# Kernel optimization log

Measured on AMD Instinct MI355X. Metric: run time of the kernel, lower is better.

The kernel has to match this reference:

```python
import jax, jax.numpy as jnp
import numpy as np

B, T, D, H = 32, 1024, 256, 256


def setup_inputs() -> dict:
    key = jax.random.key(0)
    ks = jax.random.split(key, 11)
    x = jax.random.normal(ks[0], (B, T, D), dtype=jnp.float32)
    len_x = jax.random.randint(ks[1], (B,), 1, T + 1).astype(jnp.int32)

    def xavier(k, fan_in, fan_out):
        return (jax.random.normal(k, (fan_out, fan_in)) * np.sqrt(2.0 / (fan_in + fan_out))).astype(jnp.float32)

    def unif(k, fan_in, shape):
        bound = 1.0 / np.sqrt(fan_in)
        return jax.random.uniform(k, shape, minval=-bound, maxval=bound).astype(jnp.float32)

    return {
        "x": x, "len_x": len_x,
        "Ww1_w": xavier(ks[2], D, H), "Ww1_b": unif(ks[3], D, (H,)),
        "Ww2_w": unif(ks[4], H, (D, H)), "Ww2_b": unif(ks[5], H, (D,)),
        "Wb1_w": xavier(ks[6], D, H), "Wb1_b": unif(ks[7], D, (H,)),
        "Wb2_w": unif(ks[8], H, (D, H)), "Wb2_b": unif(ks[9], H, (D,)),
    }


def _mlp(c, w1, b1, w2, b2):
    h = jax.nn.gelu(c @ w1.T + b1, approximate=False)
    return h @ w2.T + b2


def _ragged_dft(z, lengths, inverse):
    # z: [B, T, D] complex64; per-sample DFT over the first lengths[i] steps.
    t = z.shape[1]
    n = jnp.arange(t)
    kn = (n[:, None] * n[None, :]).astype(jnp.float32)          # [T, T]
    l = lengths.astype(jnp.float32)[:, None, None]               # [B, 1, 1]
    sign = 1.0 if inverse else -1.0
    ang = sign * 2.0 * jnp.pi * kn[None, :, :] / l               # [B, T, T]
    valid = n[None, :] < lengths[:, None]                        # [B, T]
    mask = (valid[:, :, None] & valid[:, None, :]).astype(jnp.float32)
    Wm = jnp.exp(1j * ang).astype(jnp.complex64) * mask
    if inverse:
        Wm = Wm / l.astype(jnp.complex64)
    return jnp.einsum("bkn,bnd->bkd", Wm, z)


def _crelu(z):
    mag = jnp.abs(z)
    phase = jnp.angle(z)
    recomposed = (mag * jnp.exp(1j * phase)).astype(jnp.complex64)
    return jnp.where(mag > 0, recomposed, jnp.zeros((), jnp.complex64))


def reference(x, len_x, Ww1_w, Ww1_b, Ww2_w, Ww2_b, Wb1_w, Wb1_b, Wb2_w, Wb2_b):
    # mean over valid length (torch sums over full T; padding assumed zero-filled contributes)
    c = jnp.sum(x, axis=1) / len_x.astype(x.dtype)[:, None]      # [B, D]
    x_freq = _ragged_dft(x.astype(jnp.complex64), len_x, inverse=False)
    W = _mlp(c, Ww1_w, Ww1_b, Ww2_w, Ww2_b).astype(jnp.complex64)  # [B, D]
    b = _mlp(c, Wb1_w, Wb1_b, Wb2_w, Wb2_b).astype(jnp.complex64)  # [B, D]
    filtered = x_freq * (1.0 + W[:, None, :]) + b[:, None, :]
    activated = _crelu(filtered)
    x_recon = _ragged_dft(activated, len_x, inverse=True)
    return x_recon.real.astype(x.dtype)
```

## Files before the change

### kernel.cpp

```cpp
#include <hip/hip_runtime.h>
#include <math.h>

#define BB 32
#define TT 1024
#define DD 256
#define NBLK1 1024
#define CHUNKS_PER_B 32


__global__ __launch_bounds__(256)
void k_partial(const float* __restrict__ x, float* __restrict__ partial) {
    __shared__ float4 red[4][64];
    const int g    = blockIdx.x;
    const int tid  = threadIdx.x;
    const int wave = tid >> 6;
    const int lane = tid & 63;
    const int row0 = g * 32;

    const float4* xr = (const float4*)(x + (size_t)(row0 + wave * 8) * DD);
    float4 s; s.x = 0.f; s.y = 0.f; s.z = 0.f; s.w = 0.f;
#pragma unroll
    for (int r = 0; r < 8; ++r) {
        float4 v = xr[(size_t)r * 64 + lane];
        s.x += v.x; s.y += v.y; s.z += v.z; s.w += v.w;
    }
    red[wave][lane] = s;
    __syncthreads();
    if (tid < 64) {
        float4 a = red[0][tid], b = red[1][tid], c = red[2][tid], d = red[3][tid];
        float4 o;
        o.x = (a.x + b.x) + (c.x + d.x);
        o.y = (a.y + b.y) + (c.y + d.y);
        o.z = (a.z + b.z) + (c.z + d.z);
        o.w = (a.w + b.w) + (c.w + d.w);
        ((float4*)(partial + (size_t)g * DD))[tid] = o;
    }
}

__global__ __launch_bounds__(256)
void k_mlp(const float* __restrict__ partial, const int* __restrict__ len,
           const float* __restrict__ Ww1_w, const float* __restrict__ Ww1_b,
           const float* __restrict__ Ww2_w, const float* __restrict__ Ww2_b,
           const float* __restrict__ Wb1_w, const float* __restrict__ Wb1_b,
           const float* __restrict__ Wb2_w, const float* __restrict__ Wb2_b,
           float* __restrict__ Wout, float* __restrict__ Bout) {
    __shared__ float csh[DD];
    __shared__ float hsh[DD];
    const int tid = threadIdx.x;
    const int b   = blockIdx.x >> 1;
    const int mlp = blockIdx.x & 1;

    {
        float s = 0.f;
        const float* pp = partial + (size_t)(b * CHUNKS_PER_B) * DD + tid;
#pragma unroll
        for (int ch = 0; ch < CHUNKS_PER_B; ++ch) s += pp[(size_t)ch * DD];
        csh[tid] = s / (float)len[b];
    }
    __syncthreads();
    const float* w1 = mlp ? Wb1_w : Ww1_w;
    const float* b1 = mlp ? Wb1_b : Ww1_b;
    const float* w2 = mlp ? Wb2_w : Ww2_w;
    const float* b2 = mlp ? Wb2_b : Ww2_b;
    float* op       = mlp ? Bout  : Wout;
    {
        const float4* wr = (const float4*)(w1 + (size_t)tid * DD);
        const float4* cc = (const float4*)csh;
        float s = 0.f;
#pragma unroll 8
        for (int k = 0; k < 64; ++k) {
            float4 w = wr[k];
            float4 c4 = cc[k];
            s += w.x * c4.x + w.y * c4.y + w.z * c4.z + w.w * c4.w;
        }
        float v = s + b1[tid];
        hsh[tid] = 0.5f * v * (1.0f + erff(v * 0.70710678118654752440f));
    }
    __syncthreads();
    {
        const float4* wr = (const float4*)(w2 + (size_t)tid * DD);
        const float4* hh = (const float4*)hsh;
        float s = 0.f;
#pragma unroll 8
        for (int k = 0; k < 64; ++k) {
            float4 w = wr[k];
            float4 h4 = hh[k];
            s += w.x * h4.x + w.y * h4.y + w.z * h4.z + w.w * h4.w;
        }
        op[b * DD + tid] = s + b2[tid];
    }
}

__global__ __launch_bounds__(256)
void k_apply(const float* __restrict__ x, const int* __restrict__ len,
             const float* __restrict__ Wf, const float* __restrict__ Bf,
             float* __restrict__ out) {
    const int row  = blockIdx.x * 4 + (threadIdx.x >> 6);
    const int lane = threadIdx.x & 63;
    const int b = row >> 10;
    const int t = row & (TT - 1);
    const int L = len[b];
    const size_t base = (size_t)row * DD;
    float4* o4 = (float4*)(out + base);
    if (t >= L) {
        float4 z; z.x = 0.f; z.y = 0.f; z.z = 0.f; z.w = 0.f;
        o4[lane] = z;
        return;
    }
    float4 x4 = ((const float4*)(x + base))[lane];
    float4 w4 = ((const float4*)(Wf + b * DD))[lane];
    float4 r;
    r.x = x4.x + w4.x * x4.x;
    r.y = x4.y + w4.y * x4.y;
    r.z = x4.z + w4.z * x4.z;
    r.w = x4.w + w4.w * x4.w;
    if (t == 0) {
        float4 b4 = ((const float4*)(Bf + b * DD))[lane];
        r.x += b4.x; r.y += b4.y; r.z += b4.z; r.w += b4.w;
    }
    o4[lane] = r;
}

extern "C" void kernel_launch(void* const* d_in, const int* in_sizes, int n_in,
                              void* d_out, int out_size, void* d_ws, size_t ws_size,
                              hipStream_t stream) {
    const float* x     = (const float*)d_in[0];
    const int*   len   = (const int*)d_in[1];
    const float* Ww1_w = (const float*)d_in[2];
    const float* Ww1_b = (const float*)d_in[3];
    const float* Ww2_w = (const float*)d_in[4];
    const float* Ww2_b = (const float*)d_in[5];
    const float* Wb1_w = (const float*)d_in[6];
    const float* Wb1_b = (const float*)d_in[7];
    const float* Wb2_w = (const float*)d_in[8];
    const float* Wb2_b = (const float*)d_in[9];
    float* out = (float*)d_out;

    float* ws      = (float*)d_ws;
    float* partial = ws;
    float* Wout    = ws + 262144;
    float* Bout    = ws + 270336;

    k_partial<<<NBLK1, 256, 0, stream>>>(x, partial);
    k_mlp<<<2 * BB, 256, 0, stream>>>(partial, len,
                                      Ww1_w, Ww1_b, Ww2_w, Ww2_b,
                                      Wb1_w, Wb1_b, Wb2_w, Wb2_b,
                                      Wout, Bout);
    k_apply<<<BB * TT / 4, 256, 0, stream>>>(x, len, Wout, Bout, out);
}
```

Baseline: 119.7 us.

## Fuse partial column sums and MLP into one kernel via flag-based inter-block sync

Merges the per-chunk reduction kernel and the MLP kernel into a single launch. Every block writes its partial sum and publishes a tagged release flag. Selected blocks (two per batch) then spin on the flags of their 32 source chunks, acquire, and run the MLP. This removes one kernel launch and its gap. In exchange it relies on all waited-on blocks being co-resident or scheduled in order, and the flags are never reset, so later calls can see stale flags from a previous run.

```diff
diff --git a/kernel.cpp b/kernel.cpp
--- a/kernel.cpp
+++ b/kernel.cpp
@@ -5,57 +5,76 @@
 #define TT 1024
 #define DD 256
 #define NBLK1 1024
-#define CHUNKS_PER_B 32
+#define CHB 32
+
+#define TAGP 0x13570000u
 
 
-__global__ __launch_bounds__(256)
-void k_partial(const float* __restrict__ x, float* __restrict__ partial) {
+__global__ __launch_bounds__(256, 4)
+void k_partial_mlp(const float* __restrict__ x, const int* __restrict__ len,
+                   const float* __restrict__ Ww1_w, const float* __restrict__ Ww1_b,
+                   const float* __restrict__ Ww2_w, const float* __restrict__ Ww2_b,
+                   const float* __restrict__ Wb1_w, const float* __restrict__ Wb1_b,
+                   const float* __restrict__ Wb2_w, const float* __restrict__ Wb2_b,
+                   float* __restrict__ partial,
+                   unsigned* __restrict__ pflag,
+                   float* __restrict__ Wout,
+                   float* __restrict__ Bout)
+{
     __shared__ float4 red[4][64];
+    __shared__ float  csh[DD];
+    __shared__ float  hsh[DD];
+
     const int g    = blockIdx.x;
     const int tid  = threadIdx.x;
     const int wave = tid >> 6;
     const int lane = tid & 63;
     const int row0 = g * 32;
 
-    const float4* xr = (const float4*)(x + (size_t)(row0 + wave * 8) * DD);
-    float4 s; s.x = 0.f; s.y = 0.f; s.z = 0.f; s.w = 0.f;
+    {
+        const float4* xr = (const float4*)(x + (size_t)(row0 + wave * 8) * DD);
+        float4 s; s.x = 0.f; s.y = 0.f; s.z = 0.f; s.w = 0.f;
 #pragma unroll
-    for (int r = 0; r < 8; ++r) {
-        float4 v = xr[(size_t)r * 64 + lane];
-        s.x += v.x; s.y += v.y; s.z += v.z; s.w += v.w;
+        for (int r = 0; r < 8; ++r) {
+            float4 v = xr[(size_t)r * 64 + lane];
+            s.x += v.x; s.y += v.y; s.z += v.z; s.w += v.w;
+        }
+        red[wave][lane] = s;
     }
-    red[wave][lane] = s;
     __syncthreads();
     if (tid < 64) {
-        float4 a = red[0][tid], b = red[1][tid], c = red[2][tid], d = red[3][tid];
+        float4 a = red[0][tid], c2 = red[1][tid], c3 = red[2][tid], c4 = red[3][tid];
         float4 o;
-        o.x = (a.x + b.x) + (c.x + d.x);
-        o.y = (a.y + b.y) + (c.y + d.y);
-        o.z = (a.z + b.z) + (c.z + d.z);
-        o.w = (a.w + b.w) + (c.w + d.w);
+        o.x = (a.x + c2.x) + (c3.x + c4.x);
+        o.y = (a.y + c2.y) + (c3.y + c4.y);
+        o.z = (a.z + c2.z) + (c3.z + c4.z);
+        o.w = (a.w + c2.w) + (c3.w + c4.w);
         ((float4*)(partial + (size_t)g * DD))[tid] = o;
+        if (tid == 0)
+            __hip_atomic_store(&pflag[g], TAGP | (unsigned)g,
+                               __ATOMIC_RELEASE, __HIP_MEMORY_SCOPE_AGENT);
     }
-}
 
-__global__ __launch_bounds__(256)
-void k_mlp(const float* __restrict__ partial, const int* __restrict__ len,
-           const float* __restrict__ Ww1_w, const float* __restrict__ Ww1_b,
-           const float* __restrict__ Ww2_w, const float* __restrict__ Ww2_b,
-           const float* __restrict__ Wb1_w, const float* __restrict__ Wb1_b,
-           const float* __restrict__ Wb2_w, const float* __restrict__ Wb2_b,
-           float* __restrict__ Wout, float* __restrict__ Bout) {
-    __shared__ float csh[DD];
-    __shared__ float hsh[DD];
-    const int tid = threadIdx.x;
-    const int b   = blockIdx.x >> 1;
-    const int mlp = blockIdx.x & 1;
+    if ((g & 15) != 0) return;
+    const int fb  = g >> 5;
+    const int mlp = (g >> 4) & 1;
+
+    if (tid < CHB) {
+        const int src = fb * CHB + tid;
+        const unsigned want = TAGP | (unsigned)src;
+        while (__hip_atomic_load(&pflag[src], __ATOMIC_RELAXED,
+                                 __HIP_MEMORY_SCOPE_AGENT) != want)
+            __builtin_amdgcn_s_sleep(4);
+    }
+    __syncthreads();
+    __builtin_amdgcn_fence(__ATOMIC_ACQUIRE, "agent");
 
     {
         float s = 0.f;
-        const float* pp = partial + (size_t)(b * CHUNKS_PER_B) * DD + tid;
+        const float* pp = partial + (size_t)(fb * CHB) * DD + tid;
 #pragma unroll
-        for (int ch = 0; ch < CHUNKS_PER_B; ++ch) s += pp[(size_t)ch * DD];
-        csh[tid] = s / (float)len[b];
+        for (int ch = 0; ch < CHB; ++ch) s += pp[(size_t)ch * DD];
+        csh[tid] = s / (float)len[fb];
     }
     __syncthreads();
     const float* w1 = mlp ? Wb1_w : Ww1_w;
@@ -87,7 +106,7 @@
             float4 h4 = hh[k];
             s += w.x * h4.x + w.y * h4.y + w.z * h4.z + w.w * h4.w;
         }
-        op[b * DD + tid] = s + b2[tid];
+        op[fb * DD + tid] = s + b2[tid];
     }
 }
 
@@ -136,15 +155,15 @@
     const float* Wb2_b = (const float*)d_in[9];
     float* out = (float*)d_out;
 
-    float* ws      = (float*)d_ws;
-    float* partial = ws;
-    float* Wout    = ws + 262144;
-    float* Bout    = ws + 270336;
+    float*    ws      = (float*)d_ws;
+    float*    partial = ws;
+    float*    Wout    = ws + 262144;
+    float*    Bout    = ws + 270336;
+    unsigned* pflag   = (unsigned*)(ws + 278528);
 
-    k_partial<<<NBLK1, 256, 0, stream>>>(x, partial);
-    k_mlp<<<2 * BB, 256, 0, stream>>>(partial, len,
-                                      Ww1_w, Ww1_b, Ww2_w, Ww2_b,
-                                      Wb1_w, Wb1_b, Wb2_w, Wb2_b,
-                                      Wout, Bout);
+    k_partial_mlp<<<NBLK1, 256, 0, stream>>>(x, len,
+                                             Ww1_w, Ww1_b, Ww2_w, Ww2_b,
+                                             Wb1_w, Wb1_b, Wb2_w, Wb2_b,
+                                             partial, pflag, Wout, Bout);
     k_apply<<<BB * TT / 4, 256, 0, stream>>>(x, len, Wout, Bout, out);
 }
```

Result: slower. 191.4 us (+59.9%).
